# Kernel optimization log

Hardware: AMD Instinct MI355X
Metric: run time of the kernel (lower is better)

## Reference

```python
import jax, jax.numpy as jnp
import numpy as np

S, B, C, H, W_SP = 2, 16, 256, 64, 64
K = 3

def setup_inputs() -> dict:
    key = jax.random.key(0)
    k1, k2 = jax.random.split(key)
    x = jax.random.normal(k1, (S, B, C, H, W_SP), dtype=jnp.float32)
    W = jax.random.normal(k2, (C, C, K, K), dtype=jnp.float32) * 0.05
    return {"x": x, "W": W}

def reference(x, W):
    shape = x.shape
    C_ = shape[-3]
    k = W.shape[-1]
    pad = k // 2
    # flatten leading dims -> (N, C, H, W)
    xf = x.reshape((-1,) + shape[-3:])
    # diagonal mask: zero out all cross-channel filters (effectively depthwise)
    eye = jnp.eye(C_, dtype=W.dtype)[:, :, None, None]
    w = W * eye
    out = jax.lax.conv_general_dilated(
        xf, w,
        window_strides=(1, 1),
        padding=[(pad, pad), (pad, pad)],
        dimension_numbers=("NCHW", "OIHW", "NCHW"),
    )
    return out.reshape(shape)
```

## Files before the change

kernel.cpp:

```cpp
#include <hip/hip_runtime.h>


#define C_CH 256
#define H_SP 64
#define W_SP 64
#define PLANE (H_SP * W_SP)
#define LROWS (H_SP + 2)

__global__ __launch_bounds__(256) void dwconv3x3_kernel(
    const float* __restrict__ x,
    const float* __restrict__ Wfull,
    float* __restrict__ out)
{
    __shared__ float tile[LROWS * W_SP];

    const int p = blockIdx.x;
    const int c = p & (C_CH - 1);
    const float* __restrict__ xp = x + (size_t)p * PLANE;
    float* __restrict__ op = out + (size_t)p * PLANE;

    const float* __restrict__ wp = Wfull + (size_t)c * (C_CH + 1) * 9;
    const float w00 = wp[0], w01 = wp[1], w02 = wp[2];
    const float w10 = wp[3], w11 = wp[4], w12 = wp[5];
    const float w20 = wp[6], w21 = wp[7], w22 = wp[8];

    const int t = threadIdx.x;

    float4* tv = (float4*)tile;
    if (t < 16)       tv[t] = make_float4(0.f, 0.f, 0.f, 0.f);
    else if (t < 32)  tv[(H_SP + 1) * 16 + (t - 16)] = make_float4(0.f, 0.f, 0.f, 0.f);

    const float4* __restrict__ xv = (const float4*)xp;
#pragma unroll
    for (int i = 0; i < 4; ++i)
        tv[16 + t + i * 256] = xv[t + i * 256];
    __syncthreads();

    const int q  = t & 15;
    const int hb = (t >> 4) << 2;
    const int w4 = q << 2;

    float4 v[6];
    float  lf[6], rt[6];
#pragma unroll
    for (int j = 0; j < 6; ++j) {
        const int row  = hb + j;
        const int base = row * W_SP;
        v[j] = tv[row * 16 + q];
        const int li = (q == 0)  ? base : (base + w4 - 1);
        const float l = tile[li];
        lf[j] = (q == 0)  ? 0.f : l;
        const int ri = (q == 15) ? base : (base + w4 + 4);
        const float r = tile[ri];
        rt[j] = (q == 15) ? 0.f : r;
    }

#pragma unroll
    for (int r = 0; r < 4; ++r) {
        float4 acc = make_float4(0.f, 0.f, 0.f, 0.f);
#pragma unroll
        for (int kh = 0; kh < 3; ++kh) {
            const int j = r + kh;
            float k0, k1, k2;
            if (kh == 0)      { k0 = w00; k1 = w01; k2 = w02; }
            else if (kh == 1) { k0 = w10; k1 = w11; k2 = w12; }
            else              { k0 = w20; k1 = w21; k2 = w22; }
            const float4 cv = v[j];
            acc.x = fmaf(lf[j], k0, fmaf(cv.x, k1, fmaf(cv.y, k2, acc.x)));
            acc.y = fmaf(cv.x, k0, fmaf(cv.y, k1, fmaf(cv.z, k2, acc.y)));
            acc.z = fmaf(cv.y, k0, fmaf(cv.z, k1, fmaf(cv.w, k2, acc.z)));
            acc.w = fmaf(cv.z, k0, fmaf(cv.w, k1, fmaf(rt[j], k2, acc.w)));
        }
        ((float4*)op)[(hb + r) * 16 + q] = acc;
    }
}

extern "C" void kernel_launch(void* const* d_in, const int* in_sizes, int n_in,
                              void* d_out, int out_size, void* d_ws, size_t ws_size,
                              hipStream_t stream) {
    const float* x = (const float*)d_in[0];
    const float* W = (const float*)d_in[1];
    float* out = (float*)d_out;

    const int n_planes = out_size / PLANE;
    dwconv3x3_kernel<<<n_planes, 256, 0, stream>>>(x, W, out);
}
```

Measured before the change: 230.5 us.

## Replace LDS tile with direct global loads, shuffles and nontemporal stores

Drops the shared-memory staging tile and the barrier. Each thread now loads its six rows (the tile row plus halo rows above and below) straight from global memory, and gets its left and right neighbours with cross-lane shuffles instead of LDS reads. Output is written with nontemporal stores so it does not pollute the cache. In exchange, halo rows are loaded twice by adjacent thread groups, which adds global/L2 traffic in place of the LDS round-trip.

```diff
diff --git a/kernel.cpp b/kernel.cpp
--- a/kernel.cpp
+++ b/kernel.cpp
@@ -5,53 +5,42 @@
 #define H_SP 64
 #define W_SP 64
 #define PLANE (H_SP * W_SP)
-#define LROWS (H_SP + 2)
+
+typedef float nfloat4 __attribute__((ext_vector_type(4)));
 
 __global__ __launch_bounds__(256) void dwconv3x3_kernel(
     const float* __restrict__ x,
     const float* __restrict__ Wfull,
     float* __restrict__ out)
 {
-    __shared__ float tile[LROWS * W_SP];
-
     const int p = blockIdx.x;
     const int c = p & (C_CH - 1);
-    const float* __restrict__ xp = x + (size_t)p * PLANE;
-    float* __restrict__ op = out + (size_t)p * PLANE;
+    const float4* __restrict__ xv = (const float4*)(x + (size_t)p * PLANE);
+    nfloat4* __restrict__ ov = (nfloat4*)(out + (size_t)p * PLANE);
 
     const float* __restrict__ wp = Wfull + (size_t)c * (C_CH + 1) * 9;
     const float w00 = wp[0], w01 = wp[1], w02 = wp[2];
     const float w10 = wp[3], w11 = wp[4], w12 = wp[5];
     const float w20 = wp[6], w21 = wp[7], w22 = wp[8];
 
-    const int t = threadIdx.x;
-
-    float4* tv = (float4*)tile;
-    if (t < 16)       tv[t] = make_float4(0.f, 0.f, 0.f, 0.f);
-    else if (t < 32)  tv[(H_SP + 1) * 16 + (t - 16)] = make_float4(0.f, 0.f, 0.f, 0.f);
-
-    const float4* __restrict__ xv = (const float4*)xp;
-#pragma unroll
-    for (int i = 0; i < 4; ++i)
-        tv[16 + t + i * 256] = xv[t + i * 256];
-    __syncthreads();
-
+    const int t  = threadIdx.x;
     const int q  = t & 15;
     const int hb = (t >> 4) << 2;
-    const int w4 = q << 2;
 
     float4 v[6];
-    float  lf[6], rt[6];
 #pragma unroll
     for (int j = 0; j < 6; ++j) {
-        const int row  = hb + j;
-        const int base = row * W_SP;
-        v[j] = tv[row * 16 + q];
-        const int li = (q == 0)  ? base : (base + w4 - 1);
-        const float l = tile[li];
-        lf[j] = (q == 0)  ? 0.f : l;
-        const int ri = (q == 15) ? base : (base + w4 + 4);
-        const float r = tile[ri];
+        const int hh = hb + j - 1;
+        v[j] = (hh >= 0 && hh < H_SP) ? xv[hh * 16 + q]
+                                      : make_float4(0.f, 0.f, 0.f, 0.f);
+    }
+
+    float lf[6], rt[6];
+#pragma unroll
+    for (int j = 0; j < 6; ++j) {
+        const float l = __shfl_up(v[j].w, 1, 64);
+        lf[j] = (q == 0) ? 0.f : l;
+        const float r = __shfl_down(v[j].x, 1, 64);
         rt[j] = (q == 15) ? 0.f : r;
     }
 
@@ -71,7 +60,8 @@
             acc.z = fmaf(cv.y, k0, fmaf(cv.z, k1, fmaf(cv.w, k2, acc.z)));
             acc.w = fmaf(cv.z, k0, fmaf(cv.w, k1, fmaf(rt[j], k2, acc.w)));
         }
-        ((float4*)op)[(hb + r) * 16 + q] = acc;
+        nfloat4 accv = { acc.x, acc.y, acc.z, acc.w };
+        __builtin_nontemporal_store(accv, &ov[(hb + r) * 16 + q]);
     }
 }
 
```

Result: no change. 233.4 us (+1.3%).
